# Optimization experiments

Hardware: AMD Instinct MI355X
Metric: run time of the kernel (lower is better)

The kernel has to match this reference:

```python
import jax, jax.numpy as jnp
import numpy as np
from jax import lax

B, S, D_IN = 4, 4096, 1024
D_FAST, D_SLOW = 512, 512
Z_BIAS_FAST, Z_BIAS_SLOW = 2.0, -2.0


def _binop(q_i, q_j):
    a_i, b_i = q_i
    a_j, b_j = q_j
    return (a_i * a_j, a_j * b_i + b_j)


def parallel_scan(a, b):
    # h_t = a_t * h_{t-1} + b_t along seq axis (axis=1)
    _, h = lax.associative_scan(_binop, (a, b), axis=1)
    return h


def setup_inputs() -> dict:
    key = jax.random.key(0)
    ks = jax.random.split(key, 6)
    scale = 0.02
    x = jax.random.normal(ks[0], (B, S, D_IN), dtype=jnp.float32)
    W_zf = jax.random.normal(ks[1], (D_IN, D_FAST), dtype=jnp.float32) * scale
    b_zf = jnp.full((D_FAST,), Z_BIAS_FAST, dtype=jnp.float32)
    W_hf = jax.random.normal(ks[2], (D_IN, D_FAST), dtype=jnp.float32) * scale
    b_hf = jnp.zeros((D_FAST,), dtype=jnp.float32)
    W_zs = jax.random.normal(ks[3], (D_IN, D_SLOW), dtype=jnp.float32) * scale
    b_zs = jnp.full((D_SLOW,), Z_BIAS_SLOW, dtype=jnp.float32)
    W_hs = jax.random.normal(ks[4], (D_IN, D_SLOW), dtype=jnp.float32) * scale
    b_hs = jnp.zeros((D_SLOW,), dtype=jnp.float32)
    W_g = jax.random.normal(ks[5], (D_FAST + D_SLOW, D_FAST + D_SLOW), dtype=jnp.float32) * scale
    b_g = jnp.zeros((D_FAST + D_SLOW,), dtype=jnp.float32)
    return {"x": x, "W_zf": W_zf, "b_zf": b_zf, "W_hf": W_hf, "b_hf": b_hf,
            "W_zs": W_zs, "b_zs": b_zs, "W_hs": W_hs, "b_hs": b_hs,
            "W_g": W_g, "b_g": b_g}


def reference(x, W_zf, b_zf, W_hf, b_hf, W_zs, b_zs, W_hs, b_hs, W_g, b_g):
    # Fast compartment (coupling='output' => slow branch sees raw x)
    z_fast = jax.nn.sigmoid(jnp.einsum('bsd,df->bsf', x, W_zf) + b_zf)
    h_tilde_fast = jnp.einsum('bsd,df->bsf', x, W_hf) + b_hf
    h_fast = parallel_scan(1.0 - z_fast, z_fast * h_tilde_fast)

    # Slow compartment
    z_slow = jax.nn.sigmoid(jnp.einsum('bsd,df->bsf', x, W_zs) + b_zs)
    h_tilde_slow = jnp.einsum('bsd,df->bsf', x, W_hs) + b_hs
    h_slow = parallel_scan(1.0 - z_slow, z_slow * h_tilde_slow)

    h_combined = jnp.concatenate([h_fast, h_slow], axis=-1)  # (B, S, D_FAST+D_SLOW)
    gate = jax.nn.sigmoid(jnp.einsum('bsc,cd->bsd', h_combined, W_g) + b_g)
    return gate * h_combined
```

## Files before the change

### kernel.cpp

```cpp
#include <hip/hip_runtime.h>

#define BB 4
#define SS 4096
#define DIN 1024
#define DH 1024
#define PN 2048
#define MM (BB*SS)
#define NC 64
#define CL 64

typedef unsigned short ushort_t;
typedef __attribute__((ext_vector_type(8))) short bf16x8;
typedef __attribute__((ext_vector_type(4))) float f32x4;
typedef __attribute__((ext_vector_type(4))) unsigned short u16x4;

__device__ inline float bf2f(ushort_t u) {
    union { float f; unsigned int i; } v; v.i = ((unsigned int)u) << 16; return v.f;
}
__device__ inline ushort_t f2bf(float f) {
    union { float f; unsigned int i; } v; v.f = f;
    unsigned int r = v.i + 0x7fffu + ((v.i >> 16) & 1u);
    return (ushort_t)(r >> 16);
}
__device__ inline float sigmoidf_(float x) { return 1.0f / (1.0f + __expf(-x)); }

__device__ inline void load_lds16(const void* g, void* l) {
    __builtin_amdgcn_global_load_lds(
        (const __attribute__((address_space(1))) void*)g,
        (__attribute__((address_space(3))) void*)l, 16, 0, 0);
}

__global__ void zero_out_kernel(float* out, int n) {
    int i = blockIdx.x * 256 + threadIdx.x;
    if (i < n) out[i] = 0.0f;
}

#define PREP_NBLK 17160
__global__ __launch_bounds__(256) void prep_kernel(
    const float* __restrict__ x,
    const float* __restrict__ Wzf, const float* __restrict__ Wzs,
    const float* __restrict__ Whf, const float* __restrict__ Whs,
    const float* __restrict__ Wg,
    const float* __restrict__ bzf, const float* __restrict__ bzs,
    const float* __restrict__ bhf, const float* __restrict__ bhs,
    ushort_t* __restrict__ WcatT, ushort_t* __restrict__ WgT,
    ushort_t* __restrict__ Xb, float* __restrict__ bcat)
{
    __shared__ ushort_t tile[64][65];
    const int bx = blockIdx.x, tid = threadIdx.x;

    if (bx < 768) {
        const float* src; ushort_t* dst; int srcN, t;
        if (bx < 512) {
            int wi = bx >> 7; t = bx & 127; srcN = 512;
            const float* S[4] = {Wzf, Wzs, Whf, Whs};
            src = S[wi];
            dst = WcatT + (size_t)(wi * 512) * DIN;
        } else {
            t = bx - 512; srcN = 1024; src = Wg; dst = WgT;
        }
        const int k0 = (t & 15) * 64, n0 = (t >> 4) * 64;
        const int tx = tid & 63, ty = tid >> 6;
        #pragma unroll
        for (int i = ty; i < 64; i += 4)
            tile[i][tx] = f2bf(src[(size_t)(k0 + i) * srcN + n0 + tx]);
        __syncthreads();
        #pragma unroll
        for (int i = ty; i < 64; i += 4)
            dst[(size_t)(n0 + i) * DIN + k0 + tx] = tile[tx][i];
    } else if (bx < 17152) {
        size_t i = ((size_t)(bx - 768) * 256 + tid) * 4;
        float4 v = *(const float4*)(x + i);
        u16x4 o;
        o.x = f2bf(v.x); o.y = f2bf(v.y); o.z = f2bf(v.z); o.w = f2bf(v.w);
        *(u16x4*)(Xb + i) = o;
    } else {
        int i = (bx - 17152) * 256 + tid;
        float v = (i < 512) ? bzf[i] : (i < 1024) ? bzs[i - 512]
                : (i < 1536) ? bhf[i - 1024] : bhs[i - 1536];
        bcat[i] = v;
    }
}

template <int EPI, int NB>
__global__ __launch_bounds__(256) void gemm_kernel(
    const ushort_t* __restrict__ A, const ushort_t* __restrict__ Bt,
    int K, int lda,
    const float* __restrict__ bias,
    ushort_t* __restrict__ Zarr, ushort_t* __restrict__ Harr,
    const float* __restrict__ bg, const ushort_t* __restrict__ Hbf,
    float* __restrict__ Out)
{
    __shared__ alignas(16) ushort_t As[128 * 64];
    __shared__ alignas(16) ushort_t Bs[128 * 64];

    const int tid  = threadIdx.x;
    const int lane = tid & 63;
    const int wave = tid >> 6;
    const int wm   = wave & 1;
    const int wn   = wave >> 1;
    const int lrow = lane & 15;
    const int kgrp = lane >> 4;

    const int id  = blockIdx.x;
    const int xcd = id & 7;
    const int s   = id >> 3;
    const int mBase = (xcd + 8 * (s / NB)) * 128;
    const int nBase = (s % NB) * 128;

    f32x4 acc[4][4] = {};

    const ushort_t* Ablk = A  + (size_t)mBase * lda;
    const ushort_t* Bblk = Bt + (size_t)nBase * K;

    for (int k0 = 0; k0 < K; k0 += 64) {
        #pragma unroll
        for (int i = 0; i < 4; i++) {
            int idx = i * 256 + tid;
            int r   = idx >> 3;
            int cc  = ((idx & 7) ^ (r & 7)) * 8;
            load_lds16(Ablk + (size_t)r * lda + k0 + cc, &As[idx * 8]);
            load_lds16(Bblk + (size_t)r * K   + k0 + cc, &Bs[idx * 8]);
        }
        __syncthreads();

        #pragma unroll
        for (int kk = 0; kk < 64; kk += 32) {
            const int c0 = (kk >> 3) + kgrp;
            bf16x8 af[4], bfr[4];
            #pragma unroll
            for (int mt = 0; mt < 4; mt++) {
                int r = wm * 64 + mt * 16 + lrow;
                af[mt] = *(const bf16x8*)&As[r * 64 + (c0 ^ (r & 7)) * 8];
            }
            #pragma unroll
            for (int nt = 0; nt < 4; nt++) {
                int r = wn * 64 + nt * 16 + lrow;
                bfr[nt] = *(const bf16x8*)&Bs[r * 64 + (c0 ^ (r & 7)) * 8];
            }
            #pragma unroll
            for (int mt = 0; mt < 4; mt++)
                #pragma unroll
                for (int nt = 0; nt < 4; nt++)
                    acc[mt][nt] = __builtin_amdgcn_mfma_f32_16x16x32_bf16(
                        af[mt], bfr[nt], acc[mt][nt], 0, 0, 0);
        }
        __syncthreads();
    }

    const int row0  = mBase + wm * 64;
    const int col0  = nBase + wn * 64;
    const int rquad = (lane >> 4) * 4;

    if (EPI == 0) {
        const bool isz = (nBase < DH);
        ushort_t* Dst  = isz ? Zarr : Harr;
        const int csub = isz ? 0 : DH;
        #pragma unroll
        for (int nt = 0; nt < 4; nt++) {
            int col  = col0 + nt * 16 + lrow;
            float bv = bias[col];
            int dcol = col - csub;
            #pragma unroll
            for (int mt = 0; mt < 4; mt++) {
                int row = row0 + mt * 16 + rquad;
                ushort_t* p = Dst + (size_t)row * DH + dcol;
                #pragma unroll
                for (int r = 0; r < 4; r++) {
                    float v = acc[mt][nt][r] + bv;
                    if (isz) v = sigmoidf_(v);
                    p[(size_t)r * DH] = f2bf(v);
                }
            }
        }
    } else {
        #pragma unroll
        for (int nt = 0; nt < 4; nt++) {
            int col  = col0 + nt * 16 + lrow;
            float bv = bg[col];
            #pragma unroll
            for (int mt = 0; mt < 4; mt++) {
                int row = row0 + mt * 16 + rquad;
                #pragma unroll
                for (int r = 0; r < 4; r++) {
                    float g = sigmoidf_(acc[mt][nt][r] + bv);
                    float h = bf2f(Hbf[(size_t)(row + r) * DH + col]);
                    Out[(size_t)(row + r) * DH + col] = g * h;
                }
            }
        }
    }
}

__global__ __launch_bounds__(256) void scan_chunk_agg(
    const ushort_t* __restrict__ Zarr, const ushort_t* __restrict__ Harr,
    float* __restrict__ Agg, float* __restrict__ Bagg)
{
    const int c4    = threadIdx.x * 4;
    const int chunk = blockIdx.x;
    const int b     = blockIdx.y;
    const size_t s0 = ((size_t)b * SS + (size_t)chunk * CL) * DH + c4;
    const ushort_t* Zp = Zarr + s0;
    const ushort_t* Hp = Harr + s0;

    float A0 = 1.0f, A1 = 1.0f, A2 = 1.0f, A3 = 1.0f;
    float B0 = 0.0f, B1 = 0.0f, B2 = 0.0f, B3 = 0.0f;
    #pragma unroll 8
    for (int t = 0; t < CL; t++) {
        u16x4 zv = *(const u16x4*)(Zp + (size_t)t * DH);
        u16x4 hv = *(const u16x4*)(Hp + (size_t)t * DH);
        float z0 = bf2f(zv.x), z1 = bf2f(zv.y), z2 = bf2f(zv.z), z3 = bf2f(zv.w);
        float h0 = bf2f(hv.x), h1 = bf2f(hv.y), h2 = bf2f(hv.z), h3 = bf2f(hv.w);
        A0 *= 1.0f - z0;  B0 = (1.0f - z0) * B0 + z0 * h0;
        A1 *= 1.0f - z1;  B1 = (1.0f - z1) * B1 + z1 * h1;
        A2 *= 1.0f - z2;  B2 = (1.0f - z2) * B2 + z2 * h2;
        A3 *= 1.0f - z3;  B3 = (1.0f - z3) * B3 + z3 * h3;
    }
    const size_t idx = ((size_t)(b * NC + chunk)) * DH + c4;
    *(float4*)(Agg  + idx) = make_float4(A0, A1, A2, A3);
    *(float4*)(Bagg + idx) = make_float4(B0, B1, B2, B3);
}

__global__ void scan_carry(const float* __restrict__ Agg, const float* __restrict__ Bagg,
                           float* __restrict__ Hinit)
{
    const int i = blockIdx.x * 256 + threadIdx.x;
    const int b = i >> 10, c = i & 1023;
    float h = 0.0f;
    for (int j = 0; j < NC; j++) {
        const size_t idx = ((size_t)(b * NC + j)) * DH + c;
        Hinit[idx] = h;
        h = Agg[idx] * h + Bagg[idx];
    }
}

__global__ __launch_bounds__(256) void scan_apply(
    const ushort_t* __restrict__ Zarr, ushort_t* Harr, const float* __restrict__ Hinit)
{
    const int c4    = threadIdx.x * 4;
    const int chunk = blockIdx.x;
    const int b     = blockIdx.y;
    const size_t s0 = ((size_t)b * SS + (size_t)chunk * CL) * DH + c4;
    const ushort_t* Zp = Zarr + s0;
    ushort_t*       Hp = Harr + s0;

    float4 hi = *(const float4*)(Hinit + ((size_t)(b * NC + chunk)) * DH + c4);
    float h0 = hi.x, h1 = hi.y, h2 = hi.z, h3 = hi.w;
    #pragma unroll 8
    for (int t = 0; t < CL; t++) {
        u16x4 zv = *(const u16x4*)(Zp + (size_t)t * DH);
        u16x4 hv = *(const u16x4*)(Hp + (size_t)t * DH);
        float z0 = bf2f(zv.x), z1 = bf2f(zv.y), z2 = bf2f(zv.z), z3 = bf2f(zv.w);
        float t0 = bf2f(hv.x), t1 = bf2f(hv.y), t2 = bf2f(hv.z), t3 = bf2f(hv.w);
        h0 = (1.0f - z0) * h0 + z0 * t0;
        h1 = (1.0f - z1) * h1 + z1 * t1;
        h2 = (1.0f - z2) * h2 + z2 * t2;
        h3 = (1.0f - z3) * h3 + z3 * t3;
        u16x4 o;
        o.x = f2bf(h0); o.y = f2bf(h1); o.z = f2bf(h2); o.w = f2bf(h3);
        *(u16x4*)(Hp + (size_t)t * DH) = o;
    }
}

extern "C" void kernel_launch(void* const* d_in, const int* in_sizes, int n_in,
                              void* d_out, int out_size, void* d_ws, size_t ws_size,
                              hipStream_t stream)
{
    const float* x   = (const float*)d_in[0];
    const float* Wzf = (const float*)d_in[1];
    const float* bzf = (const float*)d_in[2];
    const float* Whf = (const float*)d_in[3];
    const float* bhf = (const float*)d_in[4];
    const float* Wzs = (const float*)d_in[5];
    const float* bzs = (const float*)d_in[6];
    const float* Whs = (const float*)d_in[7];
    const float* bhs = (const float*)d_in[8];
    const float* Wg  = (const float*)d_in[9];
    const float* bg  = (const float*)d_in[10];

    const size_t NEED = (size_t)42 << 20;
    if (ws_size < NEED) {
        zero_out_kernel<<<(MM * DH + 255) / 256, 256, 0, stream>>>((float*)d_out, MM * DH);
        return;
    }

    char* ws = (char*)d_ws;
    ushort_t* WcatT = (ushort_t*)(ws);
    ushort_t* WgT   = (ushort_t*)(ws + ((size_t)4 << 20));
    float*    bcat  = (float*)   (ws + ((size_t)6 << 20));
    float*    Agg   = (float*)   (ws + ((size_t)6 << 20) + (64 << 10));
    float*    Bagg  = (float*)   (ws + ((size_t)7 << 20) + (64 << 10));
    float*    Hinit = (float*)   (ws + ((size_t)8 << 20) + (64 << 10));
    ushort_t* Harr  = (ushort_t*)(ws + ((size_t)10 << 20));

    ushort_t* Xb   = (ushort_t*)d_out;
    ushort_t* Zarr = Xb + (size_t)MM * DH;

    dim3 blk(256);

    prep_kernel<<<PREP_NBLK, blk, 0, stream>>>(
        x, Wzf, Wzs, Whf, Whs, Wg, bzf, bzs, bhf, bhs, WcatT, WgT, Xb, bcat);

    gemm_kernel<0, PN / 128><<<(MM / 128) * (PN / 128), blk, 0, stream>>>(
        Xb, WcatT, DIN, DIN, bcat, Zarr, Harr, nullptr, nullptr, nullptr);

    scan_chunk_agg<<<dim3(NC, BB), blk, 0, stream>>>(Zarr, Harr, Agg, Bagg);
    scan_carry<<<16, 256, 0, stream>>>(Agg, Bagg, Hinit);
    scan_apply<<<dim3(NC, BB), blk, 0, stream>>>(Zarr, Harr, Hinit);

    gemm_kernel<1, DH / 128><<<(MM / 128) * (DH / 128), blk, 0, stream>>>(
        Harr, WgT, DIN, DH, nullptr, nullptr, nullptr, bg, Harr,
        (float*)d_out);
}
```

Measured before the change: 331.0 us.

## Stage GEMM epilogues through LDS for coalesced stores and reuse staged H tile

Both GEMM epilogues now write results into a padded shared-memory tile, then store them to global memory in coalesced 16-byte vectors instead of scattered 2- or 4-byte stores. The second GEMM also captures the H values for its output columns from the A tile already in LDS at the matching k step, so the gating multiply no longer re-reads H from global memory. This adds a larger LDS footprint, extra barriers and per-thread registers for the captured values, which may lower occupancy.

Result: slower. 377.1 us (+13.9%).

```diff
diff --git a/kernel.cpp b/kernel.cpp
--- a/kernel.cpp
+++ b/kernel.cpp
@@ -11,6 +11,7 @@
 
 typedef unsigned short ushort_t;
 typedef __attribute__((ext_vector_type(8))) short bf16x8;
+typedef __attribute__((ext_vector_type(8))) unsigned short u16x8;
 typedef __attribute__((ext_vector_type(4))) float f32x4;
 typedef __attribute__((ext_vector_type(4))) unsigned short u16x4;
 
@@ -82,17 +83,16 @@
     }
 }
 
-template <int EPI, int NB>
-__global__ __launch_bounds__(256) void gemm_kernel(
+#define NB1 (PN/128)
+__global__ __launch_bounds__(256) void gemm1_mfma(
     const ushort_t* __restrict__ A, const ushort_t* __restrict__ Bt,
-    int K, int lda,
     const float* __restrict__ bias,
-    ushort_t* __restrict__ Zarr, ushort_t* __restrict__ Harr,
-    const float* __restrict__ bg, const ushort_t* __restrict__ Hbf,
-    float* __restrict__ Out)
-{
-    __shared__ alignas(16) ushort_t As[128 * 64];
-    __shared__ alignas(16) ushort_t Bs[128 * 64];
+    ushort_t* __restrict__ Zarr, ushort_t* __restrict__ Harr)
+{
+    __shared__ alignas(16) unsigned char smem[34816];
+    ushort_t* As  = (ushort_t*)smem;
+    ushort_t* Bs  = (ushort_t*)(smem + 16384);
+    ushort_t* R16 = (ushort_t*)smem;
 
     const int tid  = threadIdx.x;
     const int lane = tid & 63;
@@ -105,25 +105,23 @@
     const int id  = blockIdx.x;
     const int xcd = id & 7;
     const int s   = id >> 3;
-    const int mBase = (xcd + 8 * (s / NB)) * 128;
-    const int nBase = (s % NB) * 128;
+    const int mBase = (xcd + 8 * (s / NB1)) * 128;
+    const int nBase = (s % NB1) * 128;
 
     f32x4 acc[4][4] = {};
-
-    const ushort_t* Ablk = A  + (size_t)mBase * lda;
-    const ushort_t* Bblk = Bt + (size_t)nBase * K;
-
-    for (int k0 = 0; k0 < K; k0 += 64) {
+    const ushort_t* Ablk = A  + (size_t)mBase * DIN;
+    const ushort_t* Bblk = Bt + (size_t)nBase * DIN;
+
+    for (int k0 = 0; k0 < DIN; k0 += 64) {
         #pragma unroll
         for (int i = 0; i < 4; i++) {
             int idx = i * 256 + tid;
             int r   = idx >> 3;
             int cc  = ((idx & 7) ^ (r & 7)) * 8;
-            load_lds16(Ablk + (size_t)r * lda + k0 + cc, &As[idx * 8]);
-            load_lds16(Bblk + (size_t)r * K   + k0 + cc, &Bs[idx * 8]);
-        }
-        __syncthreads();
-
+            load_lds16(Ablk + (size_t)r * DIN + k0 + cc, &As[idx * 8]);
+            load_lds16(Bblk + (size_t)r * DIN + k0 + cc, &Bs[idx * 8]);
+        }
+        __syncthreads();
         #pragma unroll
         for (int kk = 0; kk < 64; kk += 32) {
             const int c0 = (kk >> 3) + kgrp;
@@ -148,47 +146,146 @@
         __syncthreads();
     }
 
-    const int row0  = mBase + wm * 64;
-    const int col0  = nBase + wn * 64;
+    const bool isz = (nBase < DH);
+    ushort_t* Dst  = isz ? Zarr : Harr;
+    const int dcb  = nBase - (isz ? 0 : DH);
     const int rquad = (lane >> 4) * 4;
 
-    if (EPI == 0) {
-        const bool isz = (nBase < DH);
-        ushort_t* Dst  = isz ? Zarr : Harr;
-        const int csub = isz ? 0 : DH;
-        #pragma unroll
-        for (int nt = 0; nt < 4; nt++) {
-            int col  = col0 + nt * 16 + lrow;
-            float bv = bias[col];
-            int dcol = col - csub;
-            #pragma unroll
-            for (int mt = 0; mt < 4; mt++) {
-                int row = row0 + mt * 16 + rquad;
-                ushort_t* p = Dst + (size_t)row * DH + dcol;
+    #pragma unroll
+    for (int nt = 0; nt < 4; nt++) {
+        int colrel = wn * 64 + nt * 16 + lrow;
+        float bv = bias[nBase + colrel];
+        #pragma unroll
+        for (int mt = 0; mt < 4; mt++) {
+            int rowrel = wm * 64 + mt * 16 + rquad;
+            #pragma unroll
+            for (int r = 0; r < 4; r++) {
+                float v = acc[mt][nt][r] + bv;
+                if (isz) v = sigmoidf_(v);
+                R16[(rowrel + r) * 136 + colrel] = f2bf(v);
+            }
+        }
+    }
+    __syncthreads();
+    #pragma unroll
+    for (int it = 0; it < 8; it++) {
+        int cid = it * 256 + tid;
+        int rr  = cid >> 4, cc = (cid & 15) * 8;
+        u16x8 v = *(const u16x8*)&R16[rr * 136 + cc];
+        *(u16x8*)&Dst[(size_t)(mBase + rr) * DH + dcb + cc] = v;
+    }
+}
+
+#define NB2 (DH/128)
+__global__ __launch_bounds__(256) void gemm2_mfma(
+    const ushort_t* __restrict__ A, const ushort_t* __restrict__ Bt,
+    const float* __restrict__ bg, float* __restrict__ Out)
+{
+    __shared__ alignas(16) unsigned char smem[34816];
+    ushort_t* As  = (ushort_t*)smem;
+    ushort_t* Bs  = (ushort_t*)(smem + 16384);
+    float*    R32 = (float*)smem;
+
+    const int tid  = threadIdx.x;
+    const int lane = tid & 63;
+    const int wave = tid >> 6;
+    const int wm   = wave & 1;
+    const int wn   = wave >> 1;
+    const int lrow = lane & 15;
+    const int kgrp = lane >> 4;
+    const int rquad = (lane >> 4) * 4;
+
+    const int id  = blockIdx.x;
+    const int xcd = id & 7;
+    const int s   = id >> 3;
+    const int mBase = (xcd + 8 * (s / NB2)) * 128;
+    const int nBase = (s % NB2) * 128;
+
+    f32x4 acc[4][4] = {};
+    ushort_t hcap[4][4][4];
+    const int kcap = nBase + wn * 64;
+
+    const ushort_t* Ablk = A  + (size_t)mBase * DH;
+    const ushort_t* Bblk = Bt + (size_t)nBase * DIN;
+
+    for (int k0 = 0; k0 < DIN; k0 += 64) {
+        #pragma unroll
+        for (int i = 0; i < 4; i++) {
+            int idx = i * 256 + tid;
+            int r   = idx >> 3;
+            int cc  = ((idx & 7) ^ (r & 7)) * 8;
+            load_lds16(Ablk + (size_t)r * DH  + k0 + cc, &As[idx * 8]);
+            load_lds16(Bblk + (size_t)r * DIN + k0 + cc, &Bs[idx * 8]);
+        }
+        __syncthreads();
+
+        if (k0 == kcap) {
+            #pragma unroll
+            for (int mt = 0; mt < 4; mt++)
                 #pragma unroll
                 for (int r = 0; r < 4; r++) {
-                    float v = acc[mt][nt][r] + bv;
-                    if (isz) v = sigmoidf_(v);
-                    p[(size_t)r * DH] = f2bf(v);
+                    int rrr = wm * 64 + mt * 16 + rquad + r;
+                    int sw  = rrr & 7;
+                    #pragma unroll
+                    for (int nt = 0; nt < 4; nt++) {
+                        int ck = nt * 16 + lrow;
+                        hcap[mt][nt][r] = As[rrr * 64 + (((ck >> 3) ^ sw) * 8) + (ck & 7)];
+                    }
                 }
-            }
-        }
-    } else {
-        #pragma unroll
-        for (int nt = 0; nt < 4; nt++) {
-            int col  = col0 + nt * 16 + lrow;
-            float bv = bg[col];
+        }
+
+        #pragma unroll
+        for (int kk = 0; kk < 64; kk += 32) {
+            const int c0 = (kk >> 3) + kgrp;
+            bf16x8 af[4], bfr[4];
             #pragma unroll
             for (int mt = 0; mt < 4; mt++) {
-                int row = row0 + mt * 16 + rquad;
+                int r = wm * 64 + mt * 16 + lrow;
+                af[mt] = *(const bf16x8*)&As[r * 64 + (c0 ^ (r & 7)) * 8];
+            }
+            #pragma unroll
+            for (int nt = 0; nt < 4; nt++) {
+                int r = wn * 64 + nt * 16 + lrow;
+                bfr[nt] = *(const bf16x8*)&Bs[r * 64 + (c0 ^ (r & 7)) * 8];
+            }
+            #pragma unroll
+            for (int mt = 0; mt < 4; mt++)
                 #pragma unroll
-                for (int r = 0; r < 4; r++) {
-                    float g = sigmoidf_(acc[mt][nt][r] + bv);
-                    float h = bf2f(Hbf[(size_t)(row + r) * DH + col]);
-                    Out[(size_t)(row + r) * DH + col] = g * h;
+                for (int nt = 0; nt < 4; nt++)
+                    acc[mt][nt] = __builtin_amdgcn_mfma_f32_16x16x32_bf16(
+                        af[mt], bfr[nt], acc[mt][nt], 0, 0, 0);
+        }
+        __syncthreads();
+    }
+
+    #pragma unroll
+    for (int h = 0; h < 2; h++) {
+        if (wm == h) {
+            #pragma unroll
+            for (int nt = 0; nt < 4; nt++) {
+                int colrel = wn * 64 + nt * 16 + lrow;
+                float bv = bg[nBase + colrel];
+                #pragma unroll
+                for (int mt = 0; mt < 4; mt++) {
+                    int rloc = mt * 16 + rquad;
+                    #pragma unroll
+                    for (int r = 0; r < 4; r++) {
+                        float g  = sigmoidf_(acc[mt][nt][r] + bv);
+                        float hv = bf2f(hcap[mt][nt][r]);
+                        R32[(rloc + r) * 132 + colrel] = g * hv;
+                    }
                 }
             }
         }
+        __syncthreads();
+        #pragma unroll
+        for (int it = 0; it < 8; it++) {
+            int cid = it * 256 + tid;
+            int rr  = cid >> 5, cc4 = (cid & 31) * 4;
+            float4 v = *(const float4*)&R32[rr * 132 + cc4];
+            *(float4*)&Out[(size_t)(mBase + h * 64 + rr) * DH + nBase + cc4] = v;
+        }
+        __syncthreads();
     }
 }
 
@@ -301,14 +398,11 @@
     prep_kernel<<<PREP_NBLK, blk, 0, stream>>>(
         x, Wzf, Wzs, Whf, Whs, Wg, bzf, bzs, bhf, bhs, WcatT, WgT, Xb, bcat);
 
-    gemm_kernel<0, PN / 128><<<(MM / 128) * (PN / 128), blk, 0, stream>>>(
-        Xb, WcatT, DIN, DIN, bcat, Zarr, Harr, nullptr, nullptr, nullptr);
+    gemm1_mfma<<<(MM / 128) * NB1, blk, 0, stream>>>(Xb, WcatT, bcat, Zarr, Harr);
 
     scan_chunk_agg<<<dim3(NC, BB), blk, 0, stream>>>(Zarr, Harr, Agg, Bagg);
     scan_carry<<<16, 256, 0, stream>>>(Agg, Bagg, Hinit);
     scan_apply<<<dim3(NC, BB), blk, 0, stream>>>(Zarr, Harr, Hinit);
 
-    gemm_kernel<1, DH / 128><<<(MM / 128) * (DH / 128), blk, 0, stream>>>(
-        Harr, WgT, DIN, DH, nullptr, nullptr, nullptr, bg, Harr,
-        (float*)d_out);
-}
+    gemm2_mfma<<<(MM / 128) * NB2, blk, 0, stream>>>(Harr, WgT, bg, (float*)d_out);
+}
```
